# Kernel optimization log

Hardware: AMD Instinct MI355X
Metric: run time of the kernel (lower is better)

The kernel has to match this reference:

```python
import jax, jax.numpy as jnp
import numpy as np

B, S, D, F, E, R = 16, 1024, 1024, 4096, 8, 32
LORA_ALPHA = 16
SCALING = LORA_ALPHA / R  # 0.5


def setup_inputs() -> dict:
    key = jax.random.key(0)
    ks = jax.random.split(key, 16)
    sd = 0.02
    return {
        "x": jax.random.normal(ks[0], (B, S, D), jnp.float32),
        "router_w": jax.random.normal(ks[1], (E, D), jnp.float32) * sd,
        "router_b": jnp.zeros((E,), jnp.float32),
        "fc1_w": jax.random.normal(ks[2], (F, D), jnp.float32) * sd,
        "fc1_b": jnp.zeros((F,), jnp.float32),
        "fc2_w": jax.random.normal(ks[3], (D, F), jnp.float32) * sd,
        "fc2_b": jnp.zeros((D,), jnp.float32),
        "down_A_w": jax.random.normal(ks[4], (E, R, D), jnp.float32) * sd,
        "down_A_b": jnp.zeros((E, R), jnp.float32),
        "down_B_w": jax.random.normal(ks[5], (E, F, R), jnp.float32) * sd,
        "down_B_b": jnp.zeros((E, F), jnp.float32),
        "up_A_w": jax.random.normal(ks[6], (E, R, F), jnp.float32) * sd,
        "up_A_b": jnp.zeros((E, R), jnp.float32),
        "up_B_w": jax.random.normal(ks[7], (E, D, R), jnp.float32) * sd,
        "up_B_b": jnp.zeros((E, D), jnp.float32),
    }


def _lora_moe_sparse(inp, onehot, A_w, A_b, B_w, B_b):
    # inp: [b,t,c_in]; onehot: [b,t,E] hard top-1 dispatch mask
    # h: per-expert rank activations [b,t,E,R] (small: R=32)
    h = jnp.einsum('btc,erc->bter', inp, A_w) + A_b
    g = h * onehot[..., None]  # zero out non-selected experts (sparse dispatch)
    out = jnp.einsum('bter,eor->bto', g, B_w)
    out = out + jnp.einsum('bte,eo->bto', onehot, B_b)
    return out * SCALING


def reference(x, router_w, router_b, fc1_w, fc1_b, fc2_w, fc2_b,
              down_A_w, down_A_b, down_B_w, down_B_b,
              up_A_w, up_A_b, up_B_w, up_B_b):
    # router + top-1 hard routing (straight-through expert_choice)
    logits = jnp.einsum('btd,ed->bte', x, router_w) + router_b
    routing = jax.nn.softmax(logits, axis=-1)
    idx = jnp.argmax(routing, axis=-1)                       # [b,t]
    y_hard = jax.nn.one_hot(idx, E, dtype=x.dtype)           # [b,t,E]
    expert_choice = y_hard - jax.lax.stop_gradient(routing) + routing

    # down proj: frozen fc1 + sparse LoRA combine (dropout p=0.05 -> eval/identity)
    h1 = jnp.einsum('btd,fd->btf', x, fc1_w) + fc1_b
    h1 = h1 + _lora_moe_sparse(x, y_hard, down_A_w, down_A_b, down_B_w, down_B_b)
    a = jax.nn.gelu(h1, approximate=False)

    # up proj: frozen fc2 + sparse LoRA combine
    out = jnp.einsum('btf,df->btd', a, fc2_w) + fc2_b
    out = out + _lora_moe_sparse(a, y_hard, up_A_w, up_A_b, up_B_w, up_B_b)
    return out, (routing, expert_choice)
```

## Files before the change

kernel.cpp:

```cpp
#include <hip/hip_runtime.h>
#include <hip/hip_bf16.h>
#include <math.h>


#define M_TOK 16384
#define DIM_D 1024
#define DIM_F 4096
#define NEXP 8
#define RANK 32
#define NER 256
#define K1 1280
#define K2 4352

typedef __attribute__((ext_vector_type(8))) short bf16x8;
typedef __attribute__((ext_vector_type(4))) short sh4;
typedef __attribute__((ext_vector_type(4))) float f32x4;

__device__ inline short f2bs(float x) {
  __hip_bfloat16 h = __float2bfloat16(x);
  return *reinterpret_cast<short*>(&h);
}

__device__ inline void async16(const void* g, void* l) {
  __builtin_amdgcn_global_load_lds(
      (__attribute__((address_space(1))) void*)(g),
      (__attribute__((address_space(3))) void*)(l), 16, 0, 0);
}

__device__ inline size_t pk_blk(int row, int k, int KP) {
  return (size_t)(row >> 8) * (KP >> 5) + (k >> 5);
}
__device__ inline int pk_off(int row, int k) {
  return (row & 255) * 32 + ((k & 31) ^ ((row & 8) << 1));
}

__global__ __launch_bounds__(256) void convert_packed(
    const float* __restrict__ in, short* __restrict__ out,
    int c8, int KP, int n8)
{
  const int i = blockIdx.x * 256 + threadIdx.x;
  if (i >= n8) return;
  const int row = i / c8;
  const int k = (i % c8) * 8;
  const float4* p = (const float4*)(in + (size_t)row * (c8 * 8) + k);
  float4 u = p[0], v = p[1];
  bf16x8 r;
  r[0] = f2bs(u.x); r[1] = f2bs(u.y); r[2] = f2bs(u.z); r[3] = f2bs(u.w);
  r[4] = f2bs(v.x); r[5] = f2bs(v.y); r[6] = f2bs(v.z); r[7] = f2bs(v.w);
  *(bf16x8*)(out + pk_blk(row, k, KP) * 8192 + pk_off(row, k)) = r;
}

__global__ __launch_bounds__(256) void pack_lorab(
    const float* __restrict__ in, short* __restrict__ out,
    int Nn, int KP, int ooff, int n8)
{
  const int i = blockIdx.x * 256 + threadIdx.x;
  if (i >= n8) return;
  const int e = i / (Nn * 4);
  const int rem = i % (Nn * 4);
  const int n = rem >> 2;
  const int r8 = (rem & 3) * 8;
  const int k = ooff + e * RANK + r8;
  const float4* p = (const float4*)(in + ((size_t)e * Nn + n) * RANK + r8);
  float4 u = p[0], v = p[1];
  bf16x8 r;
  r[0] = f2bs(u.x); r[1] = f2bs(u.y); r[2] = f2bs(u.z); r[3] = f2bs(u.w);
  r[4] = f2bs(v.x); r[5] = f2bs(v.y); r[6] = f2bs(v.z); r[7] = f2bs(v.w);
  *(bf16x8*)(out + pk_blk(n, k, KP) * 8192 + pk_off(n, k)) = r;
}

__global__ __launch_bounds__(256) void router_kernel(
    const float* __restrict__ X,
    const float* __restrict__ RW,
    const float* __restrict__ RB,
    float* __restrict__ routing_out,
    float* __restrict__ ec_out,
    int* __restrict__ idx_out,
    short* __restrict__ XB)
{
  const int wave = threadIdx.x >> 6;
  const int lane = threadIdx.x & 63;
  const int t = blockIdx.x * 4 + wave;

  const float4* xp = (const float4*)(X + (size_t)t * DIM_D);
  float4 xv[4];
#pragma unroll
  for (int i = 0; i < 4; ++i) xv[i] = xp[lane + 64 * i];

#pragma unroll
  for (int i = 0; i < 4; ++i) {
    sh4 o;
    o[0] = f2bs(xv[i].x); o[1] = f2bs(xv[i].y);
    o[2] = f2bs(xv[i].z); o[3] = f2bs(xv[i].w);
    const int k0 = (lane + 64 * i) * 4;
    *(sh4*)&XB[pk_blk(t, k0, K1) * 8192 + pk_off(t, k0)] = o;
  }

  float logit[NEXP];
#pragma unroll
  for (int e = 0; e < NEXP; ++e) {
    const float4* wp = (const float4*)(RW + (size_t)e * DIM_D);
    double p = 0.0;
#pragma unroll
    for (int i = 0; i < 4; ++i) {
      float4 w = wp[lane + 64 * i];
      p += (double)xv[i].x * w.x + (double)xv[i].y * w.y +
           (double)xv[i].z * w.z + (double)xv[i].w * w.w;
    }
#pragma unroll
    for (int off = 32; off > 0; off >>= 1) p += __shfl_xor(p, off);
    logit[e] = (float)p + RB[e];
  }
  float m = logit[0];
  int am = 0;
#pragma unroll
  for (int e = 1; e < NEXP; ++e)
    if (logit[e] > m) { m = logit[e]; am = e; }
  float pr[NEXP], s = 0.f;
#pragma unroll
  for (int e = 0; e < NEXP; ++e) { pr[e] = expf(logit[e] - m); s += pr[e]; }
  const float inv = 1.f / s;
  if (lane < NEXP) {
    float r = pr[lane] * inv;
    routing_out[(size_t)t * NEXP + lane] = r;
    float y = (lane == am) ? 1.f : 0.f;
    ec_out[(size_t)t * NEXP + lane] = (y - r) + r;
  }
  if (lane == 0) idx_out[t] = am;
}

template <int KM, int LDA, int OPK, int OOFF>
__global__ __launch_bounds__(256, 2) void lora_a_gemm(
    const short* __restrict__ A, const short* __restrict__ Bm,
    const float* __restrict__ bias, const int* __restrict__ idx,
    short* __restrict__ out)
{
  __shared__ __align__(16) short As[128 * 32];
  __shared__ __align__(16) short Bs[128 * 32];

  const int tid = threadIdx.x;
  const int m0 = blockIdx.y * 128;
  const int n0 = blockIdx.x * 128;
  const int lane = tid & 63;
  const int wv = tid >> 6;
  const int quad = lane >> 4;
  const int lrow = lane & 15;
  const int wr = wv >> 1;
  const int wc = wv & 1;
  const int swz = (quad * 8) ^ ((lrow & 8) << 1);

  f32x4 acc[4][4];
#pragma unroll
  for (int i = 0; i < 4; ++i)
#pragma unroll
    for (int j = 0; j < 4; ++j) acc[i][j] = (f32x4){0.f, 0.f, 0.f, 0.f};

  const short* Ab = A + ((size_t)(m0 >> 8) * (LDA >> 5)) * 8192 +
                    (size_t)(m0 & 255) * 32;
  const short* Bb = Bm + ((size_t)(n0 >> 8) * (KM >> 5)) * 8192 +
                    (size_t)(n0 & 255) * 32;

  for (int it = 0; it < KM / 32; ++it) {
    const short* a0 = Ab + (size_t)it * 8192 + tid * 8;
    const short* b0 = Bb + (size_t)it * 8192 + tid * 8;
    async16(a0, &As[tid * 8]);
    async16(a0 + 2048, &As[tid * 8 + 2048]);
    async16(b0, &Bs[tid * 8]);
    async16(b0 + 2048, &Bs[tid * 8 + 2048]);
    __syncthreads();

    bf16x8 af[4], bfv[4];
#pragma unroll
    for (int i = 0; i < 4; ++i)
      af[i] = *(const bf16x8*)&As[(wr * 64 + i * 16 + lrow) * 32 + swz];
#pragma unroll
    for (int j = 0; j < 4; ++j)
      bfv[j] = *(const bf16x8*)&Bs[(wc * 64 + j * 16 + lrow) * 32 + swz];
#pragma unroll
    for (int i = 0; i < 4; ++i)
#pragma unroll
      for (int j = 0; j < 4; ++j)
        acc[i][j] = __builtin_amdgcn_mfma_f32_16x16x32_bf16(af[i], bfv[j],
                                                            acc[i][j], 0, 0, 0);
    __syncthreads();
  }

  float cb[4];
#pragma unroll
  for (int j = 0; j < 4; ++j) cb[j] = bias[n0 + wc * 64 + j * 16 + lrow];

#pragma unroll
  for (int i = 0; i < 4; ++i) {
#pragma unroll
    for (int reg = 0; reg < 4; ++reg) {
      const int t = m0 + wr * 64 + i * 16 + quad * 4 + reg;
      const int e = idx[t];
#pragma unroll
      for (int j = 0; j < 4; ++j) {
        const int gc = n0 + wc * 64 + j * 16 + lrow;
        float v = ((gc >> 5) == e) ? 0.5f * (acc[i][j][reg] + cb[j]) : 0.f;
        const int k = OOFF + gc;
        out[pk_blk(t, k, OPK) * 8192 + pk_off(t, k)] = f2bs(v);
      }
    }
  }
}

template <int K, int N, int POUT, int EPI>
__global__ __launch_bounds__(512, 2) void gemm256(
    const short* __restrict__ A, const short* __restrict__ Bm,
    const float* __restrict__ LB, const float* __restrict__ bias,
    const int* __restrict__ idx, void* __restrict__ outv)
{
  static_assert(K % 128 == 0, "K must be multiple of 128");
  __shared__ __align__(16) short lds[65536];

  const int tid = threadIdx.x;
  const int lane = tid & 63;
  const int wv = tid >> 6;
  const int wr = wv >> 2;
  const int wc = wv & 3;
  const int quad = lane >> 4;
  const int lrow = lane & 15;

  const int gx = gridDim.x;
  int id = blockIdx.y * gx + blockIdx.x;
  const int nwg = gx * gridDim.y;
  id = (id & 7) * (nwg >> 3) + (id >> 3);
  const int m0 = (id / gx) * 256;
  const int n0 = (id % gx) * 256;

  const short* Abase = A + (size_t)(m0 >> 8) * (K >> 5) * 8192;
  const short* Bbase = Bm + (size_t)(n0 >> 8) * (K >> 5) * 8192;

  const int swz = (quad * 8) ^ ((lrow & 8) << 1);
  const int arowb = wr * 4096 + lrow * 32 + swz;
  const int browb = 16384 + wc * 2048 + lrow * 32 + swz;

  f32x4 acc[8][4];
#pragma unroll
  for (int i = 0; i < 8; ++i)
#pragma unroll
    for (int j = 0; j < 4; ++j) acc[i][j] = (f32x4){0.f, 0.f, 0.f, 0.f};

  bf16x8 af[4], bfv[4];

#define STG(base, t, h, tens, buf)                                            \
  {                                                                           \
    const short* s_ = (base) + (size_t)(2 * (t) + (h)) * 8192 + tid * 8;      \
    short* d_ = &lds[(buf)*32768 + (tens) + (h)*8192 + tid * 8];              \
    async16(s_, d_);                                                          \
    async16(s_ + 4096, d_ + 4096);                                            \
  }
#define RDB(h, buf)                                                           \
  _Pragma("unroll") for (int j = 0; j < 4; ++j)                               \
      bfv[j] = *(const bf16x8*)&lds[(buf)*32768 + (h)*8192 + browb + j * 512];
#define RDA(mh, h, buf)                                                       \
  _Pragma("unroll") for (int i = 0; i < 4; ++i)                               \
      af[i] = *(const bf16x8*)&lds[(buf)*32768 + (h)*8192 + arowb +           \
                                   (mh)*2048 + i * 512];
#define MM(mh)                                                                \
  {                                                                           \
    __builtin_amdgcn_s_setprio(1);                                            \
    _Pragma("unroll") for (int i = 0; i < 4; ++i)                             \
    _Pragma("unroll") for (int j = 0; j < 4; ++j)                             \
        acc[(mh)*4 + i][j] = __builtin_amdgcn_mfma_f32_16x16x32_bf16(         \
            af[i], bfv[j], acc[(mh)*4 + i][j], 0, 0, 0);                      \
    __builtin_amdgcn_s_setprio(0);                                            \
  }
#define BARR asm volatile("s_barrier" ::: "memory")
#define WV4 asm volatile("s_waitcnt vmcnt(4)" ::: "memory")
#define WV0 asm volatile("s_waitcnt vmcnt(0)" ::: "memory")
#define TILE(t, b, nb)                                                        \
  RDB(0, b); RDA(0, 0, b); STG(Abase, (t) + 1, 0, 0, nb);                     \
  BARR; MM(0); BARR;                                                          \
  RDA(1, 0, b); STG(Bbase, (t) + 1, 0, 16384, nb);                            \
  BARR; MM(1); WV4; BARR;                                                     \
  RDB(1, b); RDA(0, 1, b); STG(Abase, (t) + 1, 1, 0, nb);                     \
  BARR; MM(0); BARR;                                                          \
  RDA(1, 1, b); STG(Bbase, (t) + 1, 1, 16384, nb);                            \
  BARR; MM(1); WV4; BARR;

  STG(Abase, 0, 0, 0, 0);
  STG(Bbase, 0, 0, 16384, 0);
  STG(Abase, 0, 1, 0, 0);
  STG(Bbase, 0, 1, 16384, 0);
  WV4; BARR;

  constexpr int NI = K / 128;
  for (int it = 0; it < NI - 1; ++it) {
    TILE(2 * it, 0, 1);
    TILE(2 * it + 1, 1, 0);
  }
  TILE(2 * NI - 2, 0, 1);
  {
    RDB(0, 1); RDA(0, 0, 1); BARR; MM(0); BARR;
    RDA(1, 0, 1);            BARR; MM(1); WV0; BARR;
    RDB(1, 1); RDA(0, 1, 1); BARR; MM(0); BARR;
    RDA(1, 1, 1);                  MM(1);
  }
#undef STG
#undef RDB
#undef RDA
#undef MM
#undef BARR
#undef WV4
#undef WV0
#undef TILE

  const int orow0 = m0 + wr * 128;
  const int ocol0 = n0 + wc * 64;
  float cb[4];
#pragma unroll
  for (int j = 0; j < 4; ++j) cb[j] = bias[ocol0 + j * 16 + lrow];

#pragma unroll
  for (int i = 0; i < 8; ++i) {
#pragma unroll
    for (int reg = 0; reg < 4; ++reg) {
      const int t = orow0 + i * 16 + quad * 4 + reg;
      const int e = idx[t];
      const float* lbp = LB + (size_t)e * N;
#pragma unroll
      for (int j = 0; j < 4; ++j) {
        const int gc = ocol0 + j * 16 + lrow;
        float v = acc[i][j][reg] + cb[j] + 0.5f * lbp[gc];
        if (EPI == 1) {
          v = 0.5f * v * (1.0f + erff(v * 0.70710678118654752f));
          ((short*)outv)[pk_blk(t, gc, POUT) * 8192 + pk_off(t, gc)] = f2bs(v);
        } else {
          ((float*)outv)[(size_t)t * POUT + gc] = v;
        }
      }
    }
  }
}

extern "C" void kernel_launch(void* const* d_in, const int* in_sizes, int n_in,
                              void* d_out, int out_size, void* d_ws, size_t ws_size,
                              hipStream_t stream) {
  (void)in_sizes; (void)n_in; (void)out_size; (void)ws_size;
  const float* x        = (const float*)d_in[0];
  const float* router_w = (const float*)d_in[1];
  const float* router_b = (const float*)d_in[2];
  const float* fc1_w    = (const float*)d_in[3];
  const float* fc1_b    = (const float*)d_in[4];
  const float* fc2_w    = (const float*)d_in[5];
  const float* fc2_b    = (const float*)d_in[6];
  const float* down_A_w = (const float*)d_in[7];
  const float* down_A_b = (const float*)d_in[8];
  const float* down_B_w = (const float*)d_in[9];
  const float* down_B_b = (const float*)d_in[10];
  const float* up_A_w   = (const float*)d_in[11];
  const float* up_A_b   = (const float*)d_in[12];
  const float* up_B_w   = (const float*)d_in[13];
  const float* up_B_b   = (const float*)d_in[14];

  char* ws = (char*)d_ws;
  size_t off = 0;
  int* idxp  = (int*)ws;              off += (size_t)M_TOK * 4;
  short* xbw = (short*)(ws + off);    off += (size_t)M_TOK * K1 * 2;
  short* aw  = (short*)(ws + off);    off += (size_t)M_TOK * K2 * 2;
  short* B1w = (short*)(ws + off);    off += (size_t)DIM_F * K1 * 2;
  short* B2w = (short*)(ws + off);    off += (size_t)DIM_D * K2 * 2;
  short* dAb = (short*)(ws + off);    off += (size_t)NER * DIM_D * 2;
  short* uAb = (short*)(ws + off);    off += (size_t)NER * DIM_F * 2;

  float* out = (float*)d_out;
  float* routing = out + (size_t)M_TOK * DIM_D;
  float* ec = routing + (size_t)M_TOK * NEXP;

  convert_packed<<<2048, 256, 0, stream>>>(fc1_w, B1w, 128, K1, 524288);
  convert_packed<<<2048, 256, 0, stream>>>(fc2_w, B2w, 512, K2, 524288);
  convert_packed<<<128,  256, 0, stream>>>(down_A_w, dAb, 128, DIM_D, 32768);
  convert_packed<<<512,  256, 0, stream>>>(up_A_w,   uAb, 512, DIM_F, 131072);
  pack_lorab<<<512, 256, 0, stream>>>(down_B_w, B1w, DIM_F, K1, DIM_D, 131072);
  pack_lorab<<<128, 256, 0, stream>>>(up_B_w,   B2w, DIM_D, K2, DIM_F, 32768);

  router_kernel<<<M_TOK / 4, 256, 0, stream>>>(x, router_w, router_b, routing,
                                               ec, idxp, xbw);
  lora_a_gemm<DIM_D, K1, K1, DIM_D>
      <<<dim3(2, M_TOK / 128), 256, 0, stream>>>(xbw, dAb, down_A_b, idxp, xbw);
  gemm256<K1, DIM_F, K2, 1>
      <<<dim3(DIM_F / 256, M_TOK / 256), 512, 0, stream>>>(
          xbw, B1w, down_B_b, fc1_b, idxp, aw);
  lora_a_gemm<DIM_F, K2, K2, DIM_F>
      <<<dim3(2, M_TOK / 128), 256, 0, stream>>>(aw, uAb, up_A_b, idxp, aw);
  gemm256<K2, DIM_D, DIM_D, 0>
      <<<dim3(DIM_D / 256, M_TOK / 256), 512, 0, stream>>>(
          aw, B2w, up_B_b, fc2_b, idxp, out);
}
```

Measured before the change: 660.9 us.

## Replace 256x256 pipelined GEMM with unified simple 128x128 GEMM kernel

Removes the hand-scheduled double-buffered 256x256 tile GEMM and routes the main fc1/fc2 GEMMs through the simpler single-buffered 128x128 kernel previously used for the LoRA-A projections. That kernel gains grouped block-ID swizzling and higher occupancy (launch bounds 4), plus template epilogue modes for GELU-packed, fp32 and LoRA-A output. The trade is lower arithmetic intensity per tile, more A/B reloads from cache, and no explicit load/compute overlap within a block.

```diff
diff --git a/kernel.cpp b/kernel.cpp
--- a/kernel.cpp
+++ b/kernel.cpp
@@ -129,18 +129,16 @@
   if (lane == 0) idx_out[t] = am;
 }
 
-template <int KM, int LDA, int OPK, int OOFF>
-__global__ __launch_bounds__(256, 2) void lora_a_gemm(
+template <int KA, int KB, int N, int OPK, int OOFF, int EPI>
+__global__ __launch_bounds__(256, 4) void gemm128(
     const short* __restrict__ A, const short* __restrict__ Bm,
-    const float* __restrict__ bias, const int* __restrict__ idx,
-    short* __restrict__ out)
+    const float* __restrict__ LB, const float* __restrict__ bias,
+    const int* __restrict__ idx, void* __restrict__ outv)
 {
   __shared__ __align__(16) short As[128 * 32];
   __shared__ __align__(16) short Bs[128 * 32];
 
   const int tid = threadIdx.x;
-  const int m0 = blockIdx.y * 128;
-  const int n0 = blockIdx.x * 128;
   const int lane = tid & 63;
   const int wv = tid >> 6;
   const int quad = lane >> 4;
@@ -149,24 +147,31 @@
   const int wc = wv & 1;
   const int swz = (quad * 8) ^ ((lrow & 8) << 1);
 
+  const int gx = gridDim.x;
+  int id = blockIdx.y * gx + blockIdx.x;
+  const int nwg = gx * gridDim.y;
+  id = (id & 7) * (nwg >> 3) + (id >> 3);
+  const int m0 = (id / gx) * 128;
+  const int n0 = (id % gx) * 128;
+
   f32x4 acc[4][4];
 #pragma unroll
   for (int i = 0; i < 4; ++i)
 #pragma unroll
     for (int j = 0; j < 4; ++j) acc[i][j] = (f32x4){0.f, 0.f, 0.f, 0.f};
 
-  const short* Ab = A + ((size_t)(m0 >> 8) * (LDA >> 5)) * 8192 +
-                    (size_t)(m0 & 255) * 32;
-  const short* Bb = Bm + ((size_t)(n0 >> 8) * (KM >> 5)) * 8192 +
-                    (size_t)(n0 & 255) * 32;
-
-  for (int it = 0; it < KM / 32; ++it) {
-    const short* a0 = Ab + (size_t)it * 8192 + tid * 8;
-    const short* b0 = Bb + (size_t)it * 8192 + tid * 8;
-    async16(a0, &As[tid * 8]);
-    async16(a0 + 2048, &As[tid * 8 + 2048]);
-    async16(b0, &Bs[tid * 8]);
-    async16(b0 + 2048, &Bs[tid * 8 + 2048]);
+  const short* Ab = A + ((size_t)(m0 >> 8) * (KA >> 5)) * 8192 +
+                    (size_t)(m0 & 255) * 32 + tid * 8;
+  const short* Bb = Bm + ((size_t)(n0 >> 8) * (KB >> 5)) * 8192 +
+                    (size_t)(n0 & 255) * 32 + tid * 8;
+
+  for (int it = 0; it < KB / 32; ++it) {
+    async16(Ab, &As[tid * 8]);
+    async16(Ab + 2048, &As[tid * 8 + 2048]);
+    async16(Bb, &Bs[tid * 8]);
+    async16(Bb + 2048, &Bs[tid * 8 + 2048]);
+    Ab += 8192;
+    Bb += 8192;
     __syncthreads();
 
     bf16x8 af[4], bfv[4];
@@ -198,138 +203,19 @@
 #pragma unroll
       for (int j = 0; j < 4; ++j) {
         const int gc = n0 + wc * 64 + j * 16 + lrow;
-        float v = ((gc >> 5) == e) ? 0.5f * (acc[i][j][reg] + cb[j]) : 0.f;
-        const int k = OOFF + gc;
-        out[pk_blk(t, k, OPK) * 8192 + pk_off(t, k)] = f2bs(v);
-      }
-    }
-  }
-}
-
-template <int K, int N, int POUT, int EPI>
-__global__ __launch_bounds__(512, 2) void gemm256(
-    const short* __restrict__ A, const short* __restrict__ Bm,
-    const float* __restrict__ LB, const float* __restrict__ bias,
-    const int* __restrict__ idx, void* __restrict__ outv)
-{
-  static_assert(K % 128 == 0, "K must be multiple of 128");
-  __shared__ __align__(16) short lds[65536];
-
-  const int tid = threadIdx.x;
-  const int lane = tid & 63;
-  const int wv = tid >> 6;
-  const int wr = wv >> 2;
-  const int wc = wv & 3;
-  const int quad = lane >> 4;
-  const int lrow = lane & 15;
-
-  const int gx = gridDim.x;
-  int id = blockIdx.y * gx + blockIdx.x;
-  const int nwg = gx * gridDim.y;
-  id = (id & 7) * (nwg >> 3) + (id >> 3);
-  const int m0 = (id / gx) * 256;
-  const int n0 = (id % gx) * 256;
-
-  const short* Abase = A + (size_t)(m0 >> 8) * (K >> 5) * 8192;
-  const short* Bbase = Bm + (size_t)(n0 >> 8) * (K >> 5) * 8192;
-
-  const int swz = (quad * 8) ^ ((lrow & 8) << 1);
-  const int arowb = wr * 4096 + lrow * 32 + swz;
-  const int browb = 16384 + wc * 2048 + lrow * 32 + swz;
-
-  f32x4 acc[8][4];
-#pragma unroll
-  for (int i = 0; i < 8; ++i)
-#pragma unroll
-    for (int j = 0; j < 4; ++j) acc[i][j] = (f32x4){0.f, 0.f, 0.f, 0.f};
-
-  bf16x8 af[4], bfv[4];
-
-#define STG(base, t, h, tens, buf)                                            \
-  {                                                                           \
-    const short* s_ = (base) + (size_t)(2 * (t) + (h)) * 8192 + tid * 8;      \
-    short* d_ = &lds[(buf)*32768 + (tens) + (h)*8192 + tid * 8];              \
-    async16(s_, d_);                                                          \
-    async16(s_ + 4096, d_ + 4096);                                            \
-  }
-#define RDB(h, buf)                                                           \
-  _Pragma("unroll") for (int j = 0; j < 4; ++j)                               \
-      bfv[j] = *(const bf16x8*)&lds[(buf)*32768 + (h)*8192 + browb + j * 512];
-#define RDA(mh, h, buf)                                                       \
-  _Pragma("unroll") for (int i = 0; i < 4; ++i)                               \
-      af[i] = *(const bf16x8*)&lds[(buf)*32768 + (h)*8192 + arowb +           \
-                                   (mh)*2048 + i * 512];
-#define MM(mh)                                                                \
-  {                                                                           \
-    __builtin_amdgcn_s_setprio(1);                                            \
-    _Pragma("unroll") for (int i = 0; i < 4; ++i)                             \
-    _Pragma("unroll") for (int j = 0; j < 4; ++j)                             \
-        acc[(mh)*4 + i][j] = __builtin_amdgcn_mfma_f32_16x16x32_bf16(         \
-            af[i], bfv[j], acc[(mh)*4 + i][j], 0, 0, 0);                      \
-    __builtin_amdgcn_s_setprio(0);                                            \
-  }
-#define BARR asm volatile("s_barrier" ::: "memory")
-#define WV4 asm volatile("s_waitcnt vmcnt(4)" ::: "memory")
-#define WV0 asm volatile("s_waitcnt vmcnt(0)" ::: "memory")
-#define TILE(t, b, nb)                                                        \
-  RDB(0, b); RDA(0, 0, b); STG(Abase, (t) + 1, 0, 0, nb);                     \
-  BARR; MM(0); BARR;                                                          \
-  RDA(1, 0, b); STG(Bbase, (t) + 1, 0, 16384, nb);                            \
-  BARR; MM(1); WV4; BARR;                                                     \
-  RDB(1, b); RDA(0, 1, b); STG(Abase, (t) + 1, 1, 0, nb);                     \
-  BARR; MM(0); BARR;                                                          \
-  RDA(1, 1, b); STG(Bbase, (t) + 1, 1, 16384, nb);                            \
-  BARR; MM(1); WV4; BARR;
-
-  STG(Abase, 0, 0, 0, 0);
-  STG(Bbase, 0, 0, 16384, 0);
-  STG(Abase, 0, 1, 0, 0);
-  STG(Bbase, 0, 1, 16384, 0);
-  WV4; BARR;
-
-  constexpr int NI = K / 128;
-  for (int it = 0; it < NI - 1; ++it) {
-    TILE(2 * it, 0, 1);
-    TILE(2 * it + 1, 1, 0);
-  }
-  TILE(2 * NI - 2, 0, 1);
-  {
-    RDB(0, 1); RDA(0, 0, 1); BARR; MM(0); BARR;
-    RDA(1, 0, 1);            BARR; MM(1); WV0; BARR;
-    RDB(1, 1); RDA(0, 1, 1); BARR; MM(0); BARR;
-    RDA(1, 1, 1);                  MM(1);
-  }
-#undef STG
-#undef RDB
-#undef RDA
-#undef MM
-#undef BARR
-#undef WV4
-#undef WV0
-#undef TILE
-
-  const int orow0 = m0 + wr * 128;
-  const int ocol0 = n0 + wc * 64;
-  float cb[4];
-#pragma unroll
-  for (int j = 0; j < 4; ++j) cb[j] = bias[ocol0 + j * 16 + lrow];
-
-#pragma unroll
-  for (int i = 0; i < 8; ++i) {
-#pragma unroll
-    for (int reg = 0; reg < 4; ++reg) {
-      const int t = orow0 + i * 16 + quad * 4 + reg;
-      const int e = idx[t];
-      const float* lbp = LB + (size_t)e * N;
-#pragma unroll
-      for (int j = 0; j < 4; ++j) {
-        const int gc = ocol0 + j * 16 + lrow;
-        float v = acc[i][j][reg] + cb[j] + 0.5f * lbp[gc];
-        if (EPI == 1) {
-          v = 0.5f * v * (1.0f + erff(v * 0.70710678118654752f));
-          ((short*)outv)[pk_blk(t, gc, POUT) * 8192 + pk_off(t, gc)] = f2bs(v);
+        if (EPI == 2) {
+          float v = ((gc >> 5) == e) ? 0.5f * (acc[i][j][reg] + cb[j]) : 0.f;
+          const int k = OOFF + gc;
+          ((short*)outv)[pk_blk(t, k, OPK) * 8192 + pk_off(t, k)] = f2bs(v);
         } else {
-          ((float*)outv)[(size_t)t * POUT + gc] = v;
+          float v = acc[i][j][reg] + cb[j] + 0.5f * LB[(size_t)e * N + gc];
+          if (EPI == 1) {
+            v = 0.5f * v * (1.0f + erff(v * 0.70710678118654752f));
+            const int k = OOFF + gc;
+            ((short*)outv)[pk_blk(t, k, OPK) * 8192 + pk_off(t, k)] = f2bs(v);
+          } else {
+            ((float*)outv)[(size_t)t * OPK + gc] = v;
+          }
         }
       }
     }
@@ -379,14 +265,16 @@
 
   router_kernel<<<M_TOK / 4, 256, 0, stream>>>(x, router_w, router_b, routing,
                                                ec, idxp, xbw);
-  lora_a_gemm<DIM_D, K1, K1, DIM_D>
-      <<<dim3(2, M_TOK / 128), 256, 0, stream>>>(xbw, dAb, down_A_b, idxp, xbw);
-  gemm256<K1, DIM_F, K2, 1>
-      <<<dim3(DIM_F / 256, M_TOK / 256), 512, 0, stream>>>(
+  gemm128<K1, DIM_D, NER, K1, DIM_D, 2>
+      <<<dim3(2, M_TOK / 128), 256, 0, stream>>>(
+          xbw, dAb, nullptr, down_A_b, idxp, xbw);
+  gemm128<K1, K1, DIM_F, K2, 0, 1>
+      <<<dim3(DIM_F / 128, M_TOK / 128), 256, 0, stream>>>(
           xbw, B1w, down_B_b, fc1_b, idxp, aw);
-  lora_a_gemm<DIM_F, K2, K2, DIM_F>
-      <<<dim3(2, M_TOK / 128), 256, 0, stream>>>(aw, uAb, up_A_b, idxp, aw);
-  gemm256<K2, DIM_D, DIM_D, 0>
-      <<<dim3(DIM_D / 256, M_TOK / 256), 512, 0, stream>>>(
+  gemm128<K2, DIM_F, NER, K2, DIM_F, 2>
+      <<<dim3(2, M_TOK / 128), 256, 0, stream>>>(
+          aw, uAb, nullptr, up_A_b, idxp, aw);
+  gemm128<K2, K2, DIM_D, DIM_D, 0, 0>
+      <<<dim3(DIM_D / 128, M_TOK / 128), 256, 0, stream>>>(
           aw, B2w, up_B_b, fc2_b, idxp, out);
 }
```

After: 656.4 us. Within noise of the previous version (-0.7%).
